# Kernel tuning notes

Hardware: AMD Instinct MI355X
Metric: run time of the kernel (lower is better)

Reference implementation:

```python
import jax, jax.numpy as jnp
import numpy as np

NODE_IN, EDGE_IN, HID, L = 16, 8, 128, 4
N_NODES, N_EDGES = 50000, 600000
EPS = 1e-5


def setup_inputs() -> dict:
    key = jax.random.key(0)
    ks = jax.random.split(key, 20)
    def lin(k, fan_in, fan_out):
        b = 1.0 / np.sqrt(fan_in)
        kw, kb = jax.random.split(k)
        return (jax.random.uniform(kw, (fan_in, fan_out), jnp.float32, -b, b),
                jax.random.uniform(kb, (fan_out,), jnp.float32, -b, b))
    x = jax.random.normal(ks[0], (N_NODES, NODE_IN), jnp.float32)
    edge_index = jax.random.randint(ks[1], (2, N_EDGES), 0, N_NODES, jnp.int64)
    edge_attr = jax.random.normal(ks[2], (N_EDGES, EDGE_IN), jnp.float32)
    node_w, node_b = lin(ks[3], NODE_IN, HID)
    edge_w, edge_b = lin(ks[4], EDGE_IN, HID)
    lnode_w, lnode_b, ledge_w, ledge_b, adm_w, adm_b = [], [], [], [], [], []
    for l in range(L):
        w, b = lin(ks[5 + 3 * l], HID, HID); lnode_w.append(w); lnode_b.append(b)
        w, b = lin(ks[6 + 3 * l], HID, HID); ledge_w.append(w); ledge_b.append(b)
        w, b = lin(ks[7 + 3 * l], HID, 1); adm_w.append(w); adm_b.append(b)
    return {
        "x": x, "edge_index": edge_index, "edge_attr": edge_attr,
        "node_w": node_w, "node_b": node_b, "edge_w": edge_w, "edge_b": edge_b,
        "lnode_w": jnp.stack(lnode_w), "lnode_b": jnp.stack(lnode_b),
        "ledge_w": jnp.stack(ledge_w), "ledge_b": jnp.stack(ledge_b),
        "adm_w": jnp.stack(adm_w), "adm_b": jnp.stack(adm_b),
        "gamma": jnp.ones((L, HID), jnp.float32),
        "beta": jnp.zeros((L, HID), jnp.float32),
    }


def reference(x, edge_index, edge_attr, node_w, node_b, edge_w, edge_b,
              lnode_w, lnode_b, ledge_w, ledge_b, adm_w, adm_b, gamma, beta):
    N = x.shape[0]
    src, dst = edge_index[0], edge_index[1]
    h = x @ node_w + node_b              # [N, HID]
    ea = edge_attr @ edge_w + edge_b     # [E, HID]
    for l in range(lnode_w.shape[0]):
        hn = h @ lnode_w[l] + lnode_b[l]                         # lin_node
        y_mag = jax.nn.sigmoid(ea @ adm_w[l] + adm_b[l])         # [E, 1] admittance gate
        e = ea @ ledge_w[l] + ledge_b[l]                         # lin_edge
        msg = y_mag * (hn[src] + e)                              # gated message [E, HID]
        agg = jax.ops.segment_sum(msg, dst, num_segments=N)      # scatter-add
        mu = jnp.mean(agg, axis=-1, keepdims=True)
        var = jnp.mean((agg - mu) ** 2, axis=-1, keepdims=True)
        xn = (agg - mu) * jax.lax.rsqrt(var + EPS) * gamma[l] + beta[l]
        h = h + jax.nn.relu(xn)          # dropout is identity in eval mode
    return h
```

## Files before the change

kernel.cpp:

```cpp
#include <hip/hip_runtime.h>
#include <math.h>

#define N_NODES 50000
#define N_EDGES 600000
#define HID 128
#define NLAYERS 4
#define NODE_IN 16
#define EDGE_IN 8
#define LN_EPS 1e-5f
#define SCAN_BLOCKS ((N_NODES + 255) / 256)

typedef short bf16x8 __attribute__((ext_vector_type(8)));
typedef float f32x4 __attribute__((ext_vector_type(4)));

__device__ __forceinline__ float b2f(unsigned short u) {
    union { unsigned int i; float f; } v; v.i = ((unsigned int)u) << 16; return v.f;
}
__device__ __forceinline__ unsigned short f2b(float x) {
    union { float f; unsigned int i; } v; v.f = x;
    unsigned int b = v.i + 0x7FFFu + ((v.i >> 16) & 1u);
    return (unsigned short)(b >> 16);
}

__global__ void detect_i64(const int* ei, int* flag) {
    __shared__ int nz;
    if (threadIdx.x == 0) nz = 0;
    __syncthreads();
    int acc = 0;
    for (int i = threadIdx.x; i < 1024; i += blockDim.x)
        if (ei[2 * i + 1] != 0) acc = 1;
    if (acc) atomicOr(&nz, 1);
    __syncthreads();
    if (threadIdx.x == 0) *flag = (nz == 0) ? 1 : 0;
}

__device__ __forceinline__ int edge_src(const void* ei, int f, int e) {
    if (f) return (int)((const long long*)ei)[e];
    return ((const int*)ei)[e];
}
__device__ __forceinline__ int edge_dst(const void* ei, int f, int e) {
    if (f) return (int)((const long long*)ei)[N_EDGES + e];
    return ((const int*)ei)[N_EDGES + e];
}

__global__ void hist_k(const void* ei, const int* flag, int* cursor) {
    int e = blockIdx.x * blockDim.x + threadIdx.x;
    if (e >= N_EDGES) return;
    int f = *flag;
    atomicAdd(&cursor[edge_dst(ei, f, e)], 1);
}

__global__ void scan1_k(const int* __restrict__ cursor, int* __restrict__ locex,
                        int* __restrict__ partials) {
    __shared__ int sd[256];
    int t = threadIdx.x, i = blockIdx.x * 256 + t;
    int v = (i < N_NODES) ? cursor[i] : 0;
    sd[t] = v;
    __syncthreads();
    for (int off = 1; off < 256; off <<= 1) {
        int x = (t >= off) ? sd[t - off] : 0;
        __syncthreads();
        sd[t] += x;
        __syncthreads();
    }
    if (i < N_NODES) locex[i] = sd[t] - v;
    if (t == 255) partials[blockIdx.x] = sd[255];
}

__global__ void scan2_k(int* partials) {
    __shared__ int sd[256];
    int t = threadIdx.x;
    int v = (t < SCAN_BLOCKS) ? partials[t] : 0;
    sd[t] = v;
    __syncthreads();
    for (int off = 1; off < 256; off <<= 1) {
        int x = (t >= off) ? sd[t - off] : 0;
        __syncthreads();
        sd[t] += x;
        __syncthreads();
    }
    if (t < SCAN_BLOCKS) partials[t] = sd[t] - v;
    if (t == 255) partials[SCAN_BLOCKS] = sd[255];
}

__global__ void scan3_k(int* __restrict__ row_ptr, int* __restrict__ cursor,
                        const int* __restrict__ partials) {
    int i = blockIdx.x * 256 + threadIdx.x;
    if (i < N_NODES) {
        int r = row_ptr[i] + partials[blockIdx.x];
        row_ptr[i] = r;
        cursor[i] = r;
    }
    if (i == N_NODES) row_ptr[N_NODES] = partials[SCAN_BLOCKS];
}

__global__ void place_k(const void* ei, const int* flag, int* cursor,
                        int* sorted_src, int* sorted_eid) {
    int e = blockIdx.x * blockDim.x + threadIdx.x;
    if (e >= N_EDGES) return;
    int f = *flag;
    int s = edge_src(ei, f, e);
    int d = edge_dst(ei, f, e);
    int pos = atomicAdd(&cursor[d], 1);
    sorted_src[pos] = s;
    sorted_eid[pos] = e;
}

__global__ void precompute_k(const float* __restrict__ edge_w, const float* __restrict__ edge_b,
                             const float* __restrict__ ledge_w, const float* __restrict__ ledge_b,
                             const float* __restrict__ lnode_b,
                             const float* __restrict__ adm_w, const float* __restrict__ adm_b,
                             float* __restrict__ M, float* __restrict__ cb,
                             float* __restrict__ v, float* __restrict__ cgate) {
    int t = blockIdx.x * 256 + threadIdx.x;
    if (t < 4096) {
        int l = t >> 10, k = (t >> 7) & 7, ch = t & 127;
        const float* lw = ledge_w + (size_t)l * HID * HID;
        float a = 0.f;
        for (int j = 0; j < HID; ++j) a += edge_w[k * HID + j] * lw[j * HID + ch];
        M[t] = a;
    } else if (t < 4608) {
        int u = t - 4096;
        int l = u >> 7, ch = u & 127;
        const float* lw = ledge_w + (size_t)l * HID * HID;
        float a = ledge_b[l * HID + ch] + lnode_b[l * HID + ch];
        for (int j = 0; j < HID; ++j) a += edge_b[j] * lw[j * HID + ch];
        cb[u] = a;
    } else if (t < 4640) {
        int u = t - 4608;
        int l = u >> 3, k = u & 7;
        float a = 0.f;
        for (int j = 0; j < HID; ++j) a += edge_w[k * HID + j] * adm_w[l * HID + j];
        v[u] = a;
    } else if (t < 4644) {
        int l = t - 4640;
        float a = adm_b[l];
        for (int j = 0; j < HID; ++j) a += edge_b[j] * adm_w[l * HID + j];
        cgate[l] = a;
    }
}

__global__ void convertw_k(const float* __restrict__ lnode_w, unsigned short* __restrict__ Wt16) {
    int idx = blockIdx.x * 256 + threadIdx.x;
    if (idx >= NLAYERS * HID * HID) return;
    int l = idx >> 14, r = idx & 16383, n = r >> 7, k = r & 127;
    Wt16[idx] = f2b(lnode_w[(size_t)l * HID * HID + k * HID + n]);
}

__global__ __launch_bounds__(256) void node_stats_k(
    const int* __restrict__ row_ptr, const int* __restrict__ sorted_eid,
    const float* __restrict__ edge_attr, const float* __restrict__ vw,
    const float* __restrict__ cgate,
    float* __restrict__ agg8, float* __restrict__ sy_arr,
    float* __restrict__ y_sorted) {
    int lane = threadIdx.x & 63;
    int n = (blockIdx.x * 256 + threadIdx.x) >> 6;
    int es = lane >> 3, k = lane & 7;
    float v0 = vw[0 * 8 + k], v1 = vw[1 * 8 + k], v2 = vw[2 * 8 + k], v3 = vw[3 * 8 + k];
    float c0 = cgate[0], c1 = cgate[1], c2 = cgate[2], c3 = cgate[3];
    int ps = row_ptr[n], pe = row_ptr[n + 1];
    float a0 = 0.f, a1 = 0.f, a2 = 0.f, a3 = 0.f;
    float s0 = 0.f, s1 = 0.f, s2 = 0.f, s3 = 0.f;
    for (int p = ps + es; p < pe; p += 8) {
        int eid = sorted_eid[p];
        float ea = edge_attr[(size_t)eid * EDGE_IN + k];
        float t0 = ea * v0, t1 = ea * v1, t2 = ea * v2, t3 = ea * v3;
#pragma unroll
        for (int m = 1; m <= 4; m <<= 1) {
            t0 += __shfl_xor(t0, m, 64); t1 += __shfl_xor(t1, m, 64);
            t2 += __shfl_xor(t2, m, 64); t3 += __shfl_xor(t3, m, 64);
        }
        float y0 = 1.0f / (1.0f + expf(-(t0 + c0)));
        float y1 = 1.0f / (1.0f + expf(-(t1 + c1)));
        float y2 = 1.0f / (1.0f + expf(-(t2 + c2)));
        float y3 = 1.0f / (1.0f + expf(-(t3 + c3)));
        if (k < 4) {
            float yk = (k == 0) ? y0 : (k == 1) ? y1 : (k == 2) ? y2 : y3;
            y_sorted[(size_t)k * N_EDGES + p] = yk;
        }
        a0 += y0 * ea; a1 += y1 * ea; a2 += y2 * ea; a3 += y3 * ea;
        s0 += y0; s1 += y1; s2 += y2; s3 += y3;
    }
#pragma unroll
    for (int m = 8; m <= 32; m <<= 1) {
        a0 += __shfl_xor(a0, m, 64); a1 += __shfl_xor(a1, m, 64);
        a2 += __shfl_xor(a2, m, 64); a3 += __shfl_xor(a3, m, 64);
        s0 += __shfl_xor(s0, m, 64); s1 += __shfl_xor(s1, m, 64);
        s2 += __shfl_xor(s2, m, 64); s3 += __shfl_xor(s3, m, 64);
    }
    if (lane < 8) {
        agg8[((size_t)0 * N_NODES + n) * 8 + k] = a0;
        agg8[((size_t)1 * N_NODES + n) * 8 + k] = a1;
        agg8[((size_t)2 * N_NODES + n) * 8 + k] = a2;
        agg8[((size_t)3 * N_NODES + n) * 8 + k] = a3;
    }
    if (lane == 0) {
        sy_arr[(size_t)0 * N_NODES + n] = s0;
        sy_arr[(size_t)1 * N_NODES + n] = s1;
        sy_arr[(size_t)2 * N_NODES + n] = s2;
        sy_arr[(size_t)3 * N_NODES + n] = s3;
    }
}

__global__ void node_encode_k(const float* __restrict__ x, const float* __restrict__ nw,
                              const float* __restrict__ nb, float* __restrict__ h,
                              unsigned short* __restrict__ h16) {
    int idx = blockIdx.x * 256 + threadIdx.x;
    if (idx >= N_NODES * HID) return;
    int n = idx >> 7, c = idx & 127;
    float acc = nb[c];
#pragma unroll
    for (int k = 0; k < NODE_IN; ++k) acc += x[n * NODE_IN + k] * nw[k * HID + c];
    h[idx] = acc;
    h16[idx] = f2b(acc);
}

__global__ __launch_bounds__(256) void gather16_k(
    const int* __restrict__ row_ptr, const int* __restrict__ sorted_src,
    const float* __restrict__ y_l, const unsigned short* __restrict__ h16,
    unsigned int* __restrict__ gh16) {
    int lane = threadIdx.x & 63;
    int n = (blockIdx.x * 256 + threadIdx.x) >> 6;
    int ps = row_ptr[n], pe = row_ptr[n + 1];
    float a0 = 0.f, a1 = 0.f;
    int p = ps;
    for (; p + 3 < pe; p += 4) {
        int s0 = sorted_src[p], s1 = sorted_src[p + 1];
        int s2 = sorted_src[p + 2], s3 = sorted_src[p + 3];
        float y0 = y_l[p], y1 = y_l[p + 1], y2 = y_l[p + 2], y3 = y_l[p + 3];
        unsigned int v0 = *(const unsigned int*)(h16 + (size_t)s0 * HID + lane * 2);
        unsigned int v1 = *(const unsigned int*)(h16 + (size_t)s1 * HID + lane * 2);
        unsigned int v2 = *(const unsigned int*)(h16 + (size_t)s2 * HID + lane * 2);
        unsigned int v3 = *(const unsigned int*)(h16 + (size_t)s3 * HID + lane * 2);
        a0 += y0 * b2f((unsigned short)v0); a1 += y0 * b2f((unsigned short)(v0 >> 16));
        a0 += y1 * b2f((unsigned short)v1); a1 += y1 * b2f((unsigned short)(v1 >> 16));
        a0 += y2 * b2f((unsigned short)v2); a1 += y2 * b2f((unsigned short)(v2 >> 16));
        a0 += y3 * b2f((unsigned short)v3); a1 += y3 * b2f((unsigned short)(v3 >> 16));
    }
    for (; p < pe; ++p) {
        float y = y_l[p];
        unsigned int v = *(const unsigned int*)(h16 + (size_t)sorted_src[p] * HID + lane * 2);
        a0 += y * b2f((unsigned short)v);
        a1 += y * b2f((unsigned short)(v >> 16));
    }
    gh16[(size_t)n * 64 + lane] = ((unsigned int)f2b(a1) << 16) | f2b(a0);
}

__global__ __launch_bounds__(256) void mfma_ln_k(
    const unsigned short* __restrict__ gh16, const unsigned short* __restrict__ Wt16,
    const float* __restrict__ M_l, const float* __restrict__ cb_l,
    const float* __restrict__ agg8_l, const float* __restrict__ sy_l,
    const float* __restrict__ gm, const float* __restrict__ bt,
    const float* __restrict__ h_in, float* __restrict__ h_out,
    unsigned short* __restrict__ h16_out) {
    __shared__ float red[4][16][2];
    const int tid = threadIdx.x;
    const int w = tid >> 6, lane = tid & 63;
    const int g = lane >> 4, c = lane & 15;
    const int nbase = blockIdx.x * 16;
    const int cf0 = w * 2;

    bf16x8 afrag[4];
#pragma unroll
    for (int kc = 0; kc < 4; ++kc)
        afrag[kc] = *(const bf16x8*)(gh16 + (size_t)(nbase + c) * HID + kc * 32 + g * 8);

    f32x4 acc[2];
#pragma unroll
    for (int t = 0; t < 2; ++t) {
        acc[t] = (f32x4){0.f, 0.f, 0.f, 0.f};
        const unsigned short* wp = Wt16 + (size_t)((cf0 + t) * 16 + c) * HID + g * 8;
#pragma unroll
        for (int kc = 0; kc < 4; ++kc) {
            bf16x8 bfrag = *(const bf16x8*)(wp + kc * 32);
            acc[t] = __builtin_amdgcn_mfma_f32_16x16x32_bf16(afrag[kc], bfrag, acc[t], 0, 0, 0);
        }
    }

    float cbv[2], gav[2], bev[2], mv[2][8];
#pragma unroll
    for (int t = 0; t < 2; ++t) {
        int ch = (cf0 + t) * 16 + c;
        cbv[t] = cb_l[ch]; gav[t] = gm[ch]; bev[t] = bt[ch];
#pragma unroll
        for (int k = 0; k < 8; ++k) mv[t][k] = M_l[k * HID + ch];
    }
#pragma unroll
    for (int r = 0; r < 4; ++r) {
        int node = nbase + 4 * g + r;
        float sy = sy_l[node];
        float4 t0 = ((const float4*)agg8_l)[(size_t)node * 2];
        float4 t1 = ((const float4*)agg8_l)[(size_t)node * 2 + 1];
        float a8[8] = {t0.x, t0.y, t0.z, t0.w, t1.x, t1.y, t1.z, t1.w};
#pragma unroll
        for (int t = 0; t < 2; ++t) {
            float v = sy * cbv[t];
#pragma unroll
            for (int k = 0; k < 8; ++k) v += a8[k] * mv[t][k];
            acc[t][r] += v;
        }
    }

    float sx[4], sq[4];
#pragma unroll
    for (int r = 0; r < 4; ++r) {
        sx[r] = acc[0][r] + acc[1][r];
        sq[r] = acc[0][r] * acc[0][r] + acc[1][r] * acc[1][r];
    }
#pragma unroll
    for (int m = 1; m <= 8; m <<= 1) {
#pragma unroll
        for (int r = 0; r < 4; ++r) {
            sx[r] += __shfl_xor(sx[r], m, 64);
            sq[r] += __shfl_xor(sq[r], m, 64);
        }
    }
    if (c == 0) {
#pragma unroll
        for (int r = 0; r < 4; ++r) {
            red[w][4 * g + r][0] = sx[r];
            red[w][4 * g + r][1] = sq[r];
        }
    }
    __syncthreads();

#pragma unroll
    for (int r = 0; r < 4; ++r) {
        int row = 4 * g + r;
        float SX = red[0][row][0] + red[1][row][0] + red[2][row][0] + red[3][row][0];
        float SQ = red[0][row][1] + red[1][row][1] + red[2][row][1] + red[3][row][1];
        float mean = SX * (1.0f / HID);
        float var = SQ * (1.0f / HID) - mean * mean;
        float rstd = rsqrtf(var + LN_EPS);
        int node = nbase + row;
#pragma unroll
        for (int t = 0; t < 2; ++t) {
            int ch = (cf0 + t) * 16 + c;
            float d = acc[t][r] - mean;
            float o = h_in[(size_t)node * HID + ch] +
                      fmaxf(d * rstd * gav[t] + bev[t], 0.f);
            h_out[(size_t)node * HID + ch] = o;
            h16_out[(size_t)node * HID + ch] = f2b(o);
        }
    }
}

extern "C" void kernel_launch(void* const* d_in, const int* in_sizes, int n_in,
                              void* d_out, int out_size, void* d_ws, size_t ws_size,
                              hipStream_t stream) {
    const float* x         = (const float*)d_in[0];
    const void*  ei        = d_in[1];
    const float* edge_attr = (const float*)d_in[2];
    const float* node_w    = (const float*)d_in[3];
    const float* node_b    = (const float*)d_in[4];
    const float* edge_w    = (const float*)d_in[5];
    const float* edge_b    = (const float*)d_in[6];
    const float* lnode_w   = (const float*)d_in[7];
    const float* lnode_b   = (const float*)d_in[8];
    const float* ledge_w   = (const float*)d_in[9];
    const float* ledge_b   = (const float*)d_in[10];
    const float* adm_w     = (const float*)d_in[11];
    const float* adm_b     = (const float*)d_in[12];
    const float* gamma     = (const float*)d_in[13];
    const float* beta      = (const float*)d_in[14];
    float* h = (float*)d_out;

    char* wp = (char*)d_ws;
    auto alloc = [&](size_t bytes) -> void* {
        void* p = (void*)wp;
        wp += (bytes + 255) & ~(size_t)255;
        return p;
    };
    int*            flag       = (int*)alloc(256);
    int*            cursor     = (int*)alloc(sizeof(int) * N_NODES);
    int*            row_ptr    = (int*)alloc(sizeof(int) * (N_NODES + 1));
    int*            partials   = (int*)alloc(sizeof(int) * (SCAN_BLOCKS + 1));
    int*            sorted_src = (int*)alloc(sizeof(int) * N_EDGES);
    int*            sorted_eid = (int*)alloc(sizeof(int) * N_EDGES);
    float*          y_sorted   = (float*)alloc(sizeof(float) * NLAYERS * N_EDGES);
    float*          agg8       = (float*)alloc(sizeof(float) * NLAYERS * N_NODES * 8);
    float*          sy_arr     = (float*)alloc(sizeof(float) * NLAYERS * N_NODES);
    float*          Mw         = (float*)alloc(sizeof(float) * NLAYERS * 8 * HID);
    float*          cbw        = (float*)alloc(sizeof(float) * NLAYERS * HID);
    float*          vw         = (float*)alloc(sizeof(float) * NLAYERS * 8);
    float*          cgate      = (float*)alloc(sizeof(float) * NLAYERS);
    float*          hbuf       = (float*)alloc(sizeof(float) * (size_t)N_NODES * HID);
    unsigned short* h16        = (unsigned short*)alloc(sizeof(short) * (size_t)N_NODES * HID);
    unsigned short* gh16       = (unsigned short*)alloc(sizeof(short) * (size_t)N_NODES * HID);
    unsigned short* Wt16       = (unsigned short*)alloc(sizeof(short) * NLAYERS * HID * HID);
    (void)ws_size; (void)in_sizes; (void)n_in; (void)out_size;

    hipMemsetAsync(cursor, 0, sizeof(int) * N_NODES, stream);
    detect_i64<<<1, 256, 0, stream>>>((const int*)ei, flag);
    hist_k<<<(N_EDGES + 255) / 256, 256, 0, stream>>>(ei, flag, cursor);
    scan1_k<<<SCAN_BLOCKS, 256, 0, stream>>>(cursor, row_ptr, partials);
    scan2_k<<<1, 256, 0, stream>>>(partials);
    scan3_k<<<SCAN_BLOCKS, 256, 0, stream>>>(row_ptr, cursor, partials);
    place_k<<<(N_EDGES + 255) / 256, 256, 0, stream>>>(ei, flag, cursor, sorted_src, sorted_eid);
    precompute_k<<<19, 256, 0, stream>>>(edge_w, edge_b, ledge_w, ledge_b, lnode_b,
                                         adm_w, adm_b, Mw, cbw, vw, cgate);
    convertw_k<<<(NLAYERS * HID * HID + 255) / 256, 256, 0, stream>>>(lnode_w, Wt16);
    node_stats_k<<<N_NODES / 4, 256, 0, stream>>>(row_ptr, sorted_eid, edge_attr,
                                                  vw, cgate, agg8, sy_arr, y_sorted);
    node_encode_k<<<(N_NODES * HID + 255) / 256, 256, 0, stream>>>(x, node_w, node_b, h, h16);

    float* hin = h;
    float* hout = hbuf;
    for (int l = 0; l < NLAYERS; ++l) {
        gather16_k<<<N_NODES / 4, 256, 0, stream>>>(
            row_ptr, sorted_src, y_sorted + (size_t)l * N_EDGES, h16, (unsigned int*)gh16);
        mfma_ln_k<<<N_NODES / 16, 256, 0, stream>>>(
            gh16, Wt16 + (size_t)l * HID * HID,
            Mw + (size_t)l * 8 * HID, cbw + (size_t)l * HID,
            agg8 + (size_t)l * N_NODES * 8, sy_arr + (size_t)l * N_NODES,
            gamma + (size_t)l * HID, beta + (size_t)l * HID,
            hin, hout, h16);
        float* t = hin; hin = hout; hout = t;
    }
}
```

Baseline: 390.8 us.

## Split edge gate computation into a per-edge reorder kernel and batch gather loads

Adds a per-edge kernel that gathers edge attributes into CSR-sorted order with float4 loads and computes all four layer gates with one thread per edge. node_stats_k then only does coalesced reads and reductions, dropping its shuffle-based dot products and scattered per-lane loads. Separately, the gather kernel gains an 8-wide unrolled loop that issues all index and feature loads before accumulating, to raise memory-level parallelism. In exchange it adds a kernel launch, a 19 MB intermediate buffer and extra traffic, and switches the sigmoid to the faster, less precise __expf.

```diff
diff --git a/kernel.cpp b/kernel.cpp
--- a/kernel.cpp
+++ b/kernel.cpp
@@ -147,37 +147,47 @@
     Wt16[idx] = f2b(lnode_w[(size_t)l * HID * HID + k * HID + n]);
 }
 
+__global__ __launch_bounds__(256) void reorder_k(
+    const int* __restrict__ sorted_eid, const float* __restrict__ edge_attr,
+    const float* __restrict__ vw, const float* __restrict__ cgate,
+    float* __restrict__ ea_sorted, float* __restrict__ y_sorted) {
+    __shared__ float sv[36];
+    if (threadIdx.x < 32) sv[threadIdx.x] = vw[threadIdx.x];
+    else if (threadIdx.x < 36) sv[threadIdx.x] = cgate[threadIdx.x - 32];
+    __syncthreads();
+    int p = blockIdx.x * 256 + threadIdx.x;
+    if (p >= N_EDGES) return;
+    int eid = sorted_eid[p];
+    float4 a0 = ((const float4*)edge_attr)[(size_t)eid * 2];
+    float4 a1 = ((const float4*)edge_attr)[(size_t)eid * 2 + 1];
+    ((float4*)ea_sorted)[(size_t)p * 2] = a0;
+    ((float4*)ea_sorted)[(size_t)p * 2 + 1] = a1;
+#pragma unroll
+    for (int l = 0; l < NLAYERS; ++l) {
+        const float* vl = &sv[l * 8];
+        float t = sv[32 + l];
+        t += a0.x * vl[0] + a0.y * vl[1] + a0.z * vl[2] + a0.w * vl[3];
+        t += a1.x * vl[4] + a1.y * vl[5] + a1.z * vl[6] + a1.w * vl[7];
+        y_sorted[(size_t)l * N_EDGES + p] = 1.0f / (1.0f + __expf(-t));
+    }
+}
+
 __global__ __launch_bounds__(256) void node_stats_k(
-    const int* __restrict__ row_ptr, const int* __restrict__ sorted_eid,
-    const float* __restrict__ edge_attr, const float* __restrict__ vw,
-    const float* __restrict__ cgate,
-    float* __restrict__ agg8, float* __restrict__ sy_arr,
-    float* __restrict__ y_sorted) {
+    const int* __restrict__ row_ptr, const float* __restrict__ ea_sorted,
+    const float* __restrict__ y_sorted,
+    float* __restrict__ agg8, float* __restrict__ sy_arr) {
     int lane = threadIdx.x & 63;
     int n = (blockIdx.x * 256 + threadIdx.x) >> 6;
     int es = lane >> 3, k = lane & 7;
-    float v0 = vw[0 * 8 + k], v1 = vw[1 * 8 + k], v2 = vw[2 * 8 + k], v3 = vw[3 * 8 + k];
-    float c0 = cgate[0], c1 = cgate[1], c2 = cgate[2], c3 = cgate[3];
     int ps = row_ptr[n], pe = row_ptr[n + 1];
     float a0 = 0.f, a1 = 0.f, a2 = 0.f, a3 = 0.f;
     float s0 = 0.f, s1 = 0.f, s2 = 0.f, s3 = 0.f;
     for (int p = ps + es; p < pe; p += 8) {
-        int eid = sorted_eid[p];
-        float ea = edge_attr[(size_t)eid * EDGE_IN + k];
-        float t0 = ea * v0, t1 = ea * v1, t2 = ea * v2, t3 = ea * v3;
-#pragma unroll
-        for (int m = 1; m <= 4; m <<= 1) {
-            t0 += __shfl_xor(t0, m, 64); t1 += __shfl_xor(t1, m, 64);
-            t2 += __shfl_xor(t2, m, 64); t3 += __shfl_xor(t3, m, 64);
-        }
-        float y0 = 1.0f / (1.0f + expf(-(t0 + c0)));
-        float y1 = 1.0f / (1.0f + expf(-(t1 + c1)));
-        float y2 = 1.0f / (1.0f + expf(-(t2 + c2)));
-        float y3 = 1.0f / (1.0f + expf(-(t3 + c3)));
-        if (k < 4) {
-            float yk = (k == 0) ? y0 : (k == 1) ? y1 : (k == 2) ? y2 : y3;
-            y_sorted[(size_t)k * N_EDGES + p] = yk;
-        }
+        float ea = ea_sorted[(size_t)p * EDGE_IN + k];
+        float y0 = y_sorted[(size_t)0 * N_EDGES + p];
+        float y1 = y_sorted[(size_t)1 * N_EDGES + p];
+        float y2 = y_sorted[(size_t)2 * N_EDGES + p];
+        float y3 = y_sorted[(size_t)3 * N_EDGES + p];
         a0 += y0 * ea; a1 += y1 * ea; a2 += y2 * ea; a3 += y3 * ea;
         s0 += y0; s1 += y1; s2 += y2; s3 += y3;
     }
@@ -224,18 +234,35 @@
     int ps = row_ptr[n], pe = row_ptr[n + 1];
     float a0 = 0.f, a1 = 0.f;
     int p = ps;
+    for (; p + 7 < pe; p += 8) {
+        int s[8];
+        float y[8];
+        unsigned int v[8];
+#pragma unroll
+        for (int i = 0; i < 8; ++i) { s[i] = sorted_src[p + i]; y[i] = y_l[p + i]; }
+#pragma unroll
+        for (int i = 0; i < 8; ++i)
+            v[i] = *(const unsigned int*)(h16 + (size_t)s[i] * HID + lane * 2);
+#pragma unroll
+        for (int i = 0; i < 8; ++i) {
+            a0 += y[i] * b2f((unsigned short)v[i]);
+            a1 += y[i] * b2f((unsigned short)(v[i] >> 16));
+        }
+    }
     for (; p + 3 < pe; p += 4) {
-        int s0 = sorted_src[p], s1 = sorted_src[p + 1];
-        int s2 = sorted_src[p + 2], s3 = sorted_src[p + 3];
-        float y0 = y_l[p], y1 = y_l[p + 1], y2 = y_l[p + 2], y3 = y_l[p + 3];
-        unsigned int v0 = *(const unsigned int*)(h16 + (size_t)s0 * HID + lane * 2);
-        unsigned int v1 = *(const unsigned int*)(h16 + (size_t)s1 * HID + lane * 2);
-        unsigned int v2 = *(const unsigned int*)(h16 + (size_t)s2 * HID + lane * 2);
-        unsigned int v3 = *(const unsigned int*)(h16 + (size_t)s3 * HID + lane * 2);
-        a0 += y0 * b2f((unsigned short)v0); a1 += y0 * b2f((unsigned short)(v0 >> 16));
-        a0 += y1 * b2f((unsigned short)v1); a1 += y1 * b2f((unsigned short)(v1 >> 16));
-        a0 += y2 * b2f((unsigned short)v2); a1 += y2 * b2f((unsigned short)(v2 >> 16));
-        a0 += y3 * b2f((unsigned short)v3); a1 += y3 * b2f((unsigned short)(v3 >> 16));
+        int s[4];
+        float y[4];
+        unsigned int v[4];
+#pragma unroll
+        for (int i = 0; i < 4; ++i) { s[i] = sorted_src[p + i]; y[i] = y_l[p + i]; }
+#pragma unroll
+        for (int i = 0; i < 4; ++i)
+            v[i] = *(const unsigned int*)(h16 + (size_t)s[i] * HID + lane * 2);
+#pragma unroll
+        for (int i = 0; i < 4; ++i) {
+            a0 += y[i] * b2f((unsigned short)v[i]);
+            a1 += y[i] * b2f((unsigned short)(v[i] >> 16));
+        }
     }
     for (; p < pe; ++p) {
         float y = y_l[p];
@@ -377,6 +404,7 @@
     int*            partials   = (int*)alloc(sizeof(int) * (SCAN_BLOCKS + 1));
     int*            sorted_src = (int*)alloc(sizeof(int) * N_EDGES);
     int*            sorted_eid = (int*)alloc(sizeof(int) * N_EDGES);
+    float*          ea_sorted  = (float*)alloc(sizeof(float) * (size_t)N_EDGES * EDGE_IN);
     float*          y_sorted   = (float*)alloc(sizeof(float) * NLAYERS * N_EDGES);
     float*          agg8       = (float*)alloc(sizeof(float) * NLAYERS * N_NODES * 8);
     float*          sy_arr     = (float*)alloc(sizeof(float) * NLAYERS * N_NODES);
@@ -400,8 +428,10 @@
     precompute_k<<<19, 256, 0, stream>>>(edge_w, edge_b, ledge_w, ledge_b, lnode_b,
                                          adm_w, adm_b, Mw, cbw, vw, cgate);
     convertw_k<<<(NLAYERS * HID * HID + 255) / 256, 256, 0, stream>>>(lnode_w, Wt16);
-    node_stats_k<<<N_NODES / 4, 256, 0, stream>>>(row_ptr, sorted_eid, edge_attr,
-                                                  vw, cgate, agg8, sy_arr, y_sorted);
+    reorder_k<<<(N_EDGES + 255) / 256, 256, 0, stream>>>(sorted_eid, edge_attr,
+                                                         vw, cgate, ea_sorted, y_sorted);
+    node_stats_k<<<N_NODES / 4, 256, 0, stream>>>(row_ptr, ea_sorted, y_sorted,
+                                                  agg8, sy_arr);
     node_encode_k<<<(N_NODES * HID + 255) / 256, 256, 0, stream>>>(x, node_w, node_b, h, h16);
 
     float* hin = h;
```

Measured after the change: 376.8 us. 3.6% less time.
